# Kernel optimization log

Hardware: AMD Instinct MI355X
Metric: run time of the kernel (lower is better)

## Reference

```python
import jax, jax.numpy as jnp
import numpy as np

EMB = 1024
HEADS = 16
HEAD_DIM = EMB // HEADS


def setup_inputs() -> dict:
    key = jax.random.key(0)
    ks = jax.random.split(key, 12)
    B, S = 4, 2048
    scale = 1.0 / np.sqrt(EMB)
    inp = {
        'values': jax.random.normal(ks[0], (B, S, EMB), jnp.float32),
        'keys': jax.random.normal(ks[1], (B, S, EMB), jnp.float32),
        'query': jax.random.normal(ks[2], (B, S, EMB), jnp.float32),
        'Wv': jax.random.normal(ks[3], (EMB, EMB), jnp.float32) * scale,
        'bv': jnp.zeros((EMB,), jnp.float32),
        'Wk': jax.random.normal(ks[4], (EMB, EMB), jnp.float32) * scale,
        'bk': jnp.zeros((EMB,), jnp.float32),
        'Wq': jax.random.normal(ks[5], (EMB, EMB), jnp.float32) * scale,
        'bq': jnp.zeros((EMB,), jnp.float32),
        'Wo': jax.random.normal(ks[6], (EMB, EMB), jnp.float32) * scale,
        'bo': jnp.zeros((EMB,), jnp.float32),
    }
    return inp


def reference(values, keys, query, Wv, bv, Wk, bk, Wq, bq, Wo, bo):
    B, S, _ = values.shape
    # Linear projections (torch Linear: x @ W.T + b)
    v = values @ Wv.T + bv
    k = keys @ Wk.T + bk
    q = query @ Wq.T + bq
    # Reshape to (B, S, H, D) -- NOTE: original does NOT transpose heads,
    # so attention is computed across the HEAD axis per position.
    v = v.reshape(B, S, HEADS, HEAD_DIM)
    k = k.reshape(B, S, HEADS, HEAD_DIM)
    q = q.reshape(B, S, HEADS, HEAD_DIM)
    # (B,S,H,D) @ (B,S,D,H) -> (B,S,H,H) head-head scores
    scores = jnp.einsum('bshd,bsgd->bshg', q, k) * (HEAD_DIM ** -0.5)
    attn = jax.nn.softmax(scores, axis=-1)
    # (B,S,H,H) @ (B,S,H,D) -> (B,S,H,D)
    out = jnp.einsum('bshg,bsgd->bshd', attn, v)
    out = out.reshape(B, S, EMB)
    return out @ Wo.T + bo
```

## Files before the change

### kernel.cpp

```cpp
#include <hip/hip_runtime.h>
#include <stdint.h>

#define EMB 1024
#define LROW 40

typedef unsigned short u16;
typedef __attribute__((ext_vector_type(8))) unsigned short u16x8;
typedef __attribute__((ext_vector_type(8))) __bf16 bf16x8;
typedef __attribute__((ext_vector_type(4))) float f32x4;

__device__ __forceinline__ u16 f2bf(float f) {
  union { float f; uint32_t u; } x; x.f = f;
  uint32_t u = x.u;
  u += 0x7fff + ((u >> 16) & 1u);
  return (u16)(u >> 16);
}

template<int F32>
__device__ __forceinline__ u16x8 ld8(const void* p, size_t off) {
  if (F32) {
    const float4* f = (const float4*)((const float*)p + off);
    const float4 lo = f[0], hi = f[1];
    u16x8 r;
    r[0] = f2bf(lo.x); r[1] = f2bf(lo.y); r[2] = f2bf(lo.z); r[3] = f2bf(lo.w);
    r[4] = f2bf(hi.x); r[5] = f2bf(hi.y); r[6] = f2bf(hi.z); r[7] = f2bf(hi.w);
    return r;
  }
  return *(const u16x8*)((const u16*)p + off);
}

__device__ __forceinline__ void gl16(const u16* g, u16* l) {
  __builtin_amdgcn_global_load_lds(
      (const __attribute__((address_space(1))) void*)g,
      (__attribute__((address_space(3))) void*)l, 16, 0, 0);
}

__global__ __launch_bounds__(256) void cvt2_kernel(
    const float* __restrict__ a0, u16* __restrict__ b0, int n0,
    const float* __restrict__ a1, u16* __restrict__ b1, int n1)
{
  int i = blockIdx.x * 256 + threadIdx.x;
  const int stride = gridDim.x * 256;
  const int tot = n0 + n1;
  for (; i < tot; i += stride) {
    const float* src; u16* dst; int j;
    if (i < n0) { src = a0; dst = b0; j = i; }
    else        { src = a1; dst = b1; j = i - n0; }
    const float4* f = (const float4*)(src + (size_t)j * 8);
    const float4 lo = f[0], hi = f[1];
    u16x8 r;
    r[0] = f2bf(lo.x); r[1] = f2bf(lo.y); r[2] = f2bf(lo.z); r[3] = f2bf(lo.w);
    r[4] = f2bf(hi.x); r[5] = f2bf(hi.y); r[6] = f2bf(hi.z); r[7] = f2bf(hi.w);
    *(u16x8*)(dst + (size_t)j * 8) = r;
  }
}

template<int CF32>
__device__ __forceinline__ void gemm_lds_core(
    const u16* __restrict__ X, const u16* __restrict__ W,
    const float* __restrict__ Bias, void* __restrict__ C,
    int bm, int bn, int N, int K, u16* Al, u16* Bl)
{
  const int tid  = threadIdx.x;
  const int lane = tid & 63;
  const int w    = tid >> 6;
  const int wm = w >> 1, wn = w & 1;
  const int r16 = lane & 15, quad = lane >> 4;

  const int s0 = w * 64 + lane;
  const int s1 = s0 + 256;
  const int r0 = s0 >> 2, c0 = ((s0 & 3) ^ (r0 & 3)) * 8;
  const int r1 = s1 >> 2, c1 = ((s1 & 3) ^ (r1 & 3)) * 8;

  const u16* srcA0 = X + (size_t)(bm + r0) * K + c0;
  const u16* srcA1 = X + (size_t)(bm + r1) * K + c1;
  const u16* srcB0 = W + (size_t)(bn + r0) * K + c0;
  const u16* srcB1 = W + (size_t)(bn + r1) * K + c1;

  u16* dA0 = Al + (w * 64) * 8;
  u16* dA1 = dA0 + 256 * 8;
  u16* dB0 = Bl + (w * 64) * 8;
  u16* dB1 = dB0 + 256 * 8;

  const int swz = (quad ^ (r16 & 3)) * 8;
  int offA[4], offB[4];
#pragma unroll
  for (int t = 0; t < 4; t++) {
    offA[t] = (wm * 64 + t * 16 + r16) * 32 + swz;
    offB[t] = (wn * 64 + t * 16 + r16) * 32 + swz;
  }

  f32x4 acc[4][4];
#pragma unroll
  for (int i = 0; i < 4; i++)
#pragma unroll
    for (int j = 0; j < 4; j++)
      acc[i][j] = f32x4{0.f, 0.f, 0.f, 0.f};

  for (int k0 = 0; k0 < K; k0 += 32) {
    gl16(srcA0 + k0, dA0);
    gl16(srcA1 + k0, dA1);
    gl16(srcB0 + k0, dB0);
    gl16(srcB1 + k0, dB1);
    __syncthreads();

    bf16x8 a[4], b[4];
#pragma unroll
    for (int t = 0; t < 4; t++) a[t] = *(const bf16x8*)&Al[offA[t]];
#pragma unroll
    for (int t = 0; t < 4; t++) b[t] = *(const bf16x8*)&Bl[offB[t]];

#pragma unroll
    for (int tm = 0; tm < 4; tm++)
#pragma unroll
      for (int tn = 0; tn < 4; tn++)
        acc[tm][tn] = __builtin_amdgcn_mfma_f32_16x16x32_bf16(a[tm], b[tn], acc[tm][tn], 0, 0, 0);
    __syncthreads();
  }

#pragma unroll
  for (int tn = 0; tn < 4; tn++) {
    const int col = bn + wn * 64 + tn * 16 + r16;
    const float bias = Bias[col];
#pragma unroll
    for (int tm = 0; tm < 4; tm++) {
      const int row0 = bm + wm * 64 + tm * 16 + quad * 4;
#pragma unroll
      for (int r = 0; r < 4; r++) {
        const float val = acc[tm][tn][r] + bias;
        const size_t idx = (size_t)(row0 + r) * N + col;
        if (CF32) ((float*)C)[idx] = val;
        else      ((u16*)C)[idx]   = f2bf(val);
      }
    }
  }
}

__global__ __launch_bounds__(256, 3) void gemm_bf16_b16out_kernel(
    const u16* __restrict__ X, const u16* __restrict__ W,
    const float* __restrict__ B, u16* __restrict__ C, int N, int K)
{
  __shared__ __attribute__((aligned(16))) u16 Al[128 * 32];
  __shared__ __attribute__((aligned(16))) u16 Bl[128 * 32];
  gemm_lds_core<0>(X, W, B, C, blockIdx.y * 128, blockIdx.x * 128, N, K, Al, Bl);
}

__global__ __launch_bounds__(256, 3) void gemm_bf16_f32out_kernel(
    const u16* __restrict__ X, const u16* __restrict__ W,
    const float* __restrict__ B, float* __restrict__ C, int N, int K)
{
  __shared__ __attribute__((aligned(16))) u16 Al[128 * 32];
  __shared__ __attribute__((aligned(16))) u16 Bl[128 * 32];
  gemm_lds_core<1>(X, W, B, C, blockIdx.y * 128, blockIdx.x * 128, N, K, Al, Bl);
}

template<int XF32, int CF32>
__device__ __forceinline__ void gemm_core(
    const void* __restrict__ X, const float* __restrict__ W,
    const float* __restrict__ Bias, void* __restrict__ C,
    int bm, int bn, int N, int K, u16* Al, u16* Bl)
{
  const int tid  = threadIdx.x;
  const int lane = tid & 63;
  const int w    = tid >> 6;
  const int wm = w >> 1, wn = w & 1;
  const int r16 = lane & 15, quad = lane >> 4;

  const int s0 = tid, s1 = tid + 256;
  const int r0 = s0 >> 2, k0o = (s0 & 3) * 8;
  const int r1 = s1 >> 2, k1o = (s1 & 3) * 8;
  const int l0 = r0 * LROW + k0o;
  const int l1 = r1 * LROW + k1o;

  const size_t xo0 = (size_t)(bm + r0) * K + k0o;
  const size_t xo1 = (size_t)(bm + r1) * K + k1o;
  const size_t wo0 = (size_t)(bn + r0) * K + k0o;
  const size_t wo1 = (size_t)(bn + r1) * K + k1o;

  f32x4 acc[4][4];
#pragma unroll
  for (int i = 0; i < 4; i++)
#pragma unroll
    for (int j = 0; j < 4; j++)
      acc[i][j] = f32x4{0.f, 0.f, 0.f, 0.f};

  u16x8 xa = ld8<XF32>(X, xo0);
  u16x8 xb = ld8<XF32>(X, xo1);
  u16x8 wa = ld8<1>(W, wo0);
  u16x8 wb = ld8<1>(W, wo1);

  for (int k0 = 0; k0 < K; k0 += 32) {
    *(u16x8*)&Al[l0] = xa;
    *(u16x8*)&Al[l1] = xb;
    *(u16x8*)&Bl[l0] = wa;
    *(u16x8*)&Bl[l1] = wb;
    __syncthreads();

    const int kn = (k0 + 32 < K) ? (k0 + 32) : 0;
    xa = ld8<XF32>(X, xo0 + kn);
    xb = ld8<XF32>(X, xo1 + kn);
    wa = ld8<1>(W, wo0 + kn);
    wb = ld8<1>(W, wo1 + kn);

    bf16x8 a[4], b[4];
#pragma unroll
    for (int t = 0; t < 4; t++)
      a[t] = *(const bf16x8*)&Al[(wm * 64 + t * 16 + r16) * LROW + quad * 8];
#pragma unroll
    for (int t = 0; t < 4; t++)
      b[t] = *(const bf16x8*)&Bl[(wn * 64 + t * 16 + r16) * LROW + quad * 8];

#pragma unroll
    for (int tm = 0; tm < 4; tm++)
#pragma unroll
      for (int tn = 0; tn < 4; tn++)
        acc[tm][tn] = __builtin_amdgcn_mfma_f32_16x16x32_bf16(a[tm], b[tn], acc[tm][tn], 0, 0, 0);
    __syncthreads();
  }

#pragma unroll
  for (int tn = 0; tn < 4; tn++) {
    const int col = bn + wn * 64 + tn * 16 + r16;
    const float bias = Bias[col];
#pragma unroll
    for (int tm = 0; tm < 4; tm++) {
      const int row0 = bm + wm * 64 + tm * 16 + quad * 4;
#pragma unroll
      for (int r = 0; r < 4; r++) {
        const float val = acc[tm][tn][r] + bias;
        const size_t idx = (size_t)(row0 + r) * N + col;
        if (CF32) ((float*)C)[idx] = val;
        else      ((u16*)C)[idx]   = f2bf(val);
      }
    }
  }
}

__global__ __launch_bounds__(256, 2) void gemm_mixed_kernel(
    const u16* X, const float* W, const float* B, u16* C, int N, int K)
{
  __shared__ __attribute__((aligned(16))) u16 Al[128 * LROW];
  __shared__ __attribute__((aligned(16))) u16 Bl[128 * LROW];
  gemm_core<0, 0>(X, W, B, C, blockIdx.y * 128, blockIdx.x * 128, N, K, Al, Bl);
}

__global__ __launch_bounds__(256, 4) void attn_heads_kernel(
    const u16* Q, const u16* Km, const u16* V, u16* O)
{
  __shared__ __attribute__((aligned(16))) u16 P[4][16 * LROW];
  __shared__ __attribute__((aligned(16))) u16 VT[4][64 * LROW];

  const int tid = threadIdx.x, lane = tid & 63, w = tid >> 6;
  const int r16 = lane & 15, quad = lane >> 4;
  const size_t base = ((size_t)blockIdx.x * 4 + w) * EMB;

  const bf16x8 aq0 = *(const bf16x8*)&Q[base + r16 * 64 + quad * 8];
  const bf16x8 aq1 = *(const bf16x8*)&Q[base + r16 * 64 + 32 + quad * 8];
  const bf16x8 bk0 = *(const bf16x8*)&Km[base + r16 * 64 + quad * 8];
  const bf16x8 bk1 = *(const bf16x8*)&Km[base + r16 * 64 + 32 + quad * 8];

  const u16x8 v0 = *(const u16x8*)&V[base + lane * 16];
  const u16x8 v1 = *(const u16x8*)&V[base + lane * 16 + 8];
  const u16x8 z8 = {0, 0, 0, 0, 0, 0, 0, 0};
  *(u16x8*)&VT[w][lane * LROW + 16] = z8;
  *(u16x8*)&VT[w][lane * LROW + 24] = z8;
  const int g = lane >> 2, dbase = (lane & 3) * 16;
#pragma unroll
  for (int i = 0; i < 8; i++) {
    VT[w][(dbase + i) * LROW + g]     = v0[i];
    VT[w][(dbase + 8 + i) * LROW + g] = v1[i];
  }

  f32x4 s = f32x4{0.f, 0.f, 0.f, 0.f};
  s = __builtin_amdgcn_mfma_f32_16x16x32_bf16(aq0, bk0, s, 0, 0, 0);
  s = __builtin_amdgcn_mfma_f32_16x16x32_bf16(aq1, bk1, s, 0, 0, 0);

  float p[4];
#pragma unroll
  for (int r = 0; r < 4; r++) {
    float v = s[r] * 0.125f;
    float m = v;
#pragma unroll
    for (int d = 8; d; d >>= 1) m = fmaxf(m, __shfl_xor(m, d, 16));
    float e = __expf(v - m);
    float sum = e;
#pragma unroll
    for (int d = 8; d; d >>= 1) sum += __shfl_xor(sum, d, 16);
    p[r] = e / sum;
  }

#pragma unroll
  for (int r = 0; r < 4; r++) {
    P[w][(quad * 4 + r) * LROW + r16]      = f2bf(p[r]);
    P[w][(quad * 4 + r) * LROW + 16 + r16] = 0;
  }
  __syncthreads();

  const bf16x8 pa = *(const bf16x8*)&P[w][r16 * LROW + quad * 8];

#pragma unroll
  for (int c = 0; c < 4; c++) {
    const bf16x8 bv = *(const bf16x8*)&VT[w][(c * 16 + r16) * LROW + quad * 8];
    f32x4 o = f32x4{0.f, 0.f, 0.f, 0.f};
    o = __builtin_amdgcn_mfma_f32_16x16x32_bf16(pa, bv, o, 0, 0, 0);
#pragma unroll
    for (int r = 0; r < 4; r++)
      O[base + (size_t)(quad * 4 + r) * 64 + c * 16 + r16] = f2bf(o[r]);
  }
}

extern "C" void kernel_launch(void* const* d_in, const int* in_sizes, int n_in,
                              void* d_out, int out_size, void* d_ws, size_t ws_size,
                              hipStream_t stream)
{
  const float* values = (const float*)d_in[0];
  const float* keys   = (const float*)d_in[1];
  const float* query  = (const float*)d_in[2];
  const float* Wv = (const float*)d_in[3];
  const float* bv = (const float*)d_in[4];
  const float* Wk = (const float*)d_in[5];
  const float* bk = (const float*)d_in[6];
  const float* Wq = (const float*)d_in[7];
  const float* bq = (const float*)d_in[8];
  const float* Wo = (const float*)d_in[9];
  const float* bo = (const float*)d_in[10];

  const int M = in_sizes[0] / EMB;
  const int N = EMB, K = EMB;

  u16* q    = (u16*)d_ws;
  u16* kbuf = q + (size_t)M * EMB;
  u16* v    = (u16*)d_out;
  u16* xbuf = v + (size_t)M * EMB;
  u16* ao   = q;
  u16* wqb  = kbuf;
  u16* wvb  = kbuf + (size_t)EMB * EMB;
  u16* wob  = kbuf;

  const int n8X = M * EMB / 8;
  const int n8W = EMB * EMB / 8;

  dim3 blk(256, 1, 1);
  dim3 cg(2048, 1, 1);
  dim3 gg(N / 128, M / 128, 1);

  hipLaunchKernelGGL(cvt2_kernel, cg, blk, 0, stream, query, xbuf, n8X, Wq, wqb, n8W);
  hipLaunchKernelGGL(gemm_bf16_b16out_kernel, gg, blk, 0, stream, xbuf, wqb, bq, q, N, K);
  hipLaunchKernelGGL(cvt2_kernel, cg, blk, 0, stream, values, xbuf, n8X, Wv, wvb, n8W);
  hipLaunchKernelGGL(gemm_bf16_b16out_kernel, gg, blk, 0, stream, xbuf, wvb, bv, v, N, K);
  hipLaunchKernelGGL(cvt2_kernel, cg, blk, 0, stream, keys, xbuf, n8X,
                     (const float*)nullptr, (u16*)nullptr, 0);
  hipLaunchKernelGGL(gemm_mixed_kernel, gg, blk, 0, stream, xbuf, Wk, bk, kbuf, N, K);
  hipLaunchKernelGGL(attn_heads_kernel, dim3(M / 4, 1, 1), blk, 0, stream, q, kbuf, v, ao);
  hipLaunchKernelGGL(cvt2_kernel, cg, blk, 0, stream, Wo, wob, n8W,
                     (const float*)nullptr, (u16*)nullptr, 0);
  hipLaunchKernelGGL(gemm_bf16_f32out_kernel, gg, blk, 0, stream, ao, wob, bo, (float*)d_out, N, K);
}
```

Baseline: 313.4 us.

## Fuse QKV projections into one launch with in-kernel fp32 activation conversion

Replaces the three separate activation-conversion passes and three projection GEMMs with one weight-conversion kernel and a single QKV GEMM launch (grid z selects V/K/Q). The fused GEMM reads fp32 activations directly and converts them to bf16 while staging into swizzled LDS, and loads bf16 weights through direct global-to-LDS loads. This removes the full bf16 activation round trips through memory and several launches, and triples the GEMM grid for better occupancy. Wo conversion is batched into the same launch when workspace allows. The cost is doubled fp32 activation read bandwidth in the GEMM and extra conversion ALU work in the main loop.

Measured after the change: 298.2 us. -4.9%, faster.

```diff
diff --git a/kernel.cpp b/kernel.cpp
--- a/kernel.cpp
+++ b/kernel.cpp
@@ -16,17 +16,11 @@
   return (u16)(u >> 16);
 }
 
-template<int F32>
-__device__ __forceinline__ u16x8 ld8(const void* p, size_t off) {
-  if (F32) {
-    const float4* f = (const float4*)((const float*)p + off);
-    const float4 lo = f[0], hi = f[1];
-    u16x8 r;
-    r[0] = f2bf(lo.x); r[1] = f2bf(lo.y); r[2] = f2bf(lo.z); r[3] = f2bf(lo.w);
-    r[4] = f2bf(hi.x); r[5] = f2bf(hi.y); r[6] = f2bf(hi.z); r[7] = f2bf(hi.w);
-    return r;
-  }
-  return *(const u16x8*)((const u16*)p + off);
+__device__ __forceinline__ bf16x8 cvt8(float4 a, float4 b) {
+  bf16x8 r;
+  r[0] = (__bf16)a.x; r[1] = (__bf16)a.y; r[2] = (__bf16)a.z; r[3] = (__bf16)a.w;
+  r[4] = (__bf16)b.x; r[5] = (__bf16)b.y; r[6] = (__bf16)b.z; r[7] = (__bf16)b.w;
+  return r;
 }
 
 __device__ __forceinline__ void gl16(const u16* g, u16* l) {
@@ -35,40 +29,138 @@
       (__attribute__((address_space(3))) void*)l, 16, 0, 0);
 }
 
-__global__ __launch_bounds__(256) void cvt2_kernel(
-    const float* __restrict__ a0, u16* __restrict__ b0, int n0,
-    const float* __restrict__ a1, u16* __restrict__ b1, int n1)
-{
-  int i = blockIdx.x * 256 + threadIdx.x;
-  const int stride = gridDim.x * 256;
-  const int tot = n0 + n1;
-  for (; i < tot; i += stride) {
-    const float* src; u16* dst; int j;
-    if (i < n0) { src = a0; dst = b0; j = i; }
-    else        { src = a1; dst = b1; j = i - n0; }
-    const float4* f = (const float4*)(src + (size_t)j * 8);
-    const float4 lo = f[0], hi = f[1];
-    u16x8 r;
-    r[0] = f2bf(lo.x); r[1] = f2bf(lo.y); r[2] = f2bf(lo.z); r[3] = f2bf(lo.w);
-    r[4] = f2bf(hi.x); r[5] = f2bf(hi.y); r[6] = f2bf(hi.z); r[7] = f2bf(hi.w);
-    *(u16x8*)(dst + (size_t)j * 8) = r;
-  }
-}
-
-template<int CF32>
-__device__ __forceinline__ void gemm_lds_core(
-    const u16* __restrict__ X, const u16* __restrict__ W,
-    const float* __restrict__ Bias, void* __restrict__ C,
-    int bm, int bn, int N, int K, u16* Al, u16* Bl)
-{
+__global__ __launch_bounds__(256) void cvtw_kernel(
+    const float* __restrict__ s0, u16* __restrict__ d0,
+    const float* __restrict__ s1, u16* __restrict__ d1,
+    const float* __restrict__ s2, u16* __restrict__ d2,
+    const float* __restrict__ s3, u16* __restrict__ d3)
+{
+  const float* s; u16* d;
+  switch (blockIdx.y) {
+    case 0:  s = s0; d = d0; break;
+    case 1:  s = s1; d = d1; break;
+    case 2:  s = s2; d = d2; break;
+    default: s = s3; d = d3; break;
+  }
+  const size_t i = (size_t)blockIdx.x * 256 + threadIdx.x;
+  const float4* f = (const float4*)(s + i * 8);
+  const float4 lo = f[0], hi = f[1];
+  *(bf16x8*)(d + i * 8) = cvt8(lo, hi);
+}
+
+__global__ __launch_bounds__(256, 3) void qkv_fused_kernel(
+    const float* __restrict__ Vx, const float* __restrict__ Kx,
+    const float* __restrict__ Qx, const u16* __restrict__ Wb,
+    const float* __restrict__ Bv, const float* __restrict__ Bk,
+    const float* __restrict__ Bq,
+    u16* __restrict__ cv, u16* __restrict__ ck, u16* __restrict__ cq,
+    int N, int K)
+{
+  __shared__ __attribute__((aligned(16))) u16 Al[128 * 32];
+  __shared__ __attribute__((aligned(16))) u16 Bl[128 * 32];
+
+  const float* X; const u16* W; const float* Bias; u16* C;
+  switch (blockIdx.z) {
+    case 0:  X = Vx; W = Wb;                   Bias = Bv; C = cv; break;
+    case 1:  X = Kx; W = Wb + EMB * EMB;       Bias = Bk; C = ck; break;
+    default: X = Qx; W = Wb + 2 * EMB * EMB;   Bias = Bq; C = cq; break;
+  }
+
   const int tid  = threadIdx.x;
   const int lane = tid & 63;
   const int w    = tid >> 6;
   const int wm = w >> 1, wn = w & 1;
   const int r16 = lane & 15, quad = lane >> 4;
-
-  const int s0 = w * 64 + lane;
-  const int s1 = s0 + 256;
+  const int bm = blockIdx.y * 128, bn = blockIdx.x * 128;
+
+  const int s0 = tid, s1 = tid + 256;
+  const int r0 = s0 >> 2, c0 = s0 & 3;
+  const int r1 = s1 >> 2, c1 = s1 & 3;
+  const int lA0 = r0 * 32 + ((c0 ^ (r0 & 3)) * 8);
+  const int lA1 = r1 * 32 + ((c1 ^ (r1 & 3)) * 8);
+  const size_t xo0 = (size_t)(bm + r0) * K + c0 * 8;
+  const size_t xo1 = (size_t)(bm + r1) * K + c1 * 8;
+
+  const int bs0 = w * 64 + lane, bs1 = bs0 + 256;
+  const int br0 = bs0 >> 2, bc0 = ((bs0 & 3) ^ (br0 & 3)) * 8;
+  const int br1 = bs1 >> 2, bc1 = ((bs1 & 3) ^ (br1 & 3)) * 8;
+  const u16* srcB0 = W + (size_t)(bn + br0) * K + bc0;
+  const u16* srcB1 = W + (size_t)(bn + br1) * K + bc1;
+  u16* dB0 = Bl + (w * 64) * 8;
+  u16* dB1 = dB0 + 256 * 8;
+
+  const int swz = (quad ^ (r16 & 3)) * 8;
+  int offA[4], offB[4];
+#pragma unroll
+  for (int t = 0; t < 4; t++) {
+    offA[t] = (wm * 64 + t * 16 + r16) * 32 + swz;
+    offB[t] = (wn * 64 + t * 16 + r16) * 32 + swz;
+  }
+
+  f32x4 acc[4][4];
+#pragma unroll
+  for (int i = 0; i < 4; i++)
+#pragma unroll
+    for (int j = 0; j < 4; j++)
+      acc[i][j] = f32x4{0.f, 0.f, 0.f, 0.f};
+
+  float4 xa0 = *(const float4*)(X + xo0), xa1 = *(const float4*)(X + xo0 + 4);
+  float4 xb0 = *(const float4*)(X + xo1), xb1 = *(const float4*)(X + xo1 + 4);
+
+  for (int k0 = 0; k0 < K; k0 += 32) {
+    *(bf16x8*)&Al[lA0] = cvt8(xa0, xa1);
+    *(bf16x8*)&Al[lA1] = cvt8(xb0, xb1);
+    gl16(srcB0 + k0, dB0);
+    gl16(srcB1 + k0, dB1);
+    __syncthreads();
+
+    const int kn = (k0 + 32 < K) ? (k0 + 32) : 0;
+    xa0 = *(const float4*)(X + xo0 + kn); xa1 = *(const float4*)(X + xo0 + kn + 4);
+    xb0 = *(const float4*)(X + xo1 + kn); xb1 = *(const float4*)(X + xo1 + kn + 4);
+
+    bf16x8 a[4], b[4];
+#pragma unroll
+    for (int t = 0; t < 4; t++) a[t] = *(const bf16x8*)&Al[offA[t]];
+#pragma unroll
+    for (int t = 0; t < 4; t++) b[t] = *(const bf16x8*)&Bl[offB[t]];
+
+#pragma unroll
+    for (int tm = 0; tm < 4; tm++)
+#pragma unroll
+      for (int tn = 0; tn < 4; tn++)
+        acc[tm][tn] = __builtin_amdgcn_mfma_f32_16x16x32_bf16(a[tm], b[tn], acc[tm][tn], 0, 0, 0);
+    __syncthreads();
+  }
+
+#pragma unroll
+  for (int tn = 0; tn < 4; tn++) {
+    const int col = bn + wn * 64 + tn * 16 + r16;
+    const float bias = Bias[col];
+#pragma unroll
+    for (int tm = 0; tm < 4; tm++) {
+      const int row0 = bm + wm * 64 + tm * 16 + quad * 4;
+#pragma unroll
+      for (int r = 0; r < 4; r++)
+        C[(size_t)(row0 + r) * N + col] = f2bf(acc[tm][tn][r] + bias);
+    }
+  }
+}
+
+__global__ __launch_bounds__(256, 3) void out_gemm_kernel(
+    const u16* __restrict__ X, const u16* __restrict__ W,
+    const float* __restrict__ Bias, float* __restrict__ C, int N, int K)
+{
+  __shared__ __attribute__((aligned(16))) u16 Al[128 * 32];
+  __shared__ __attribute__((aligned(16))) u16 Bl[128 * 32];
+
+  const int tid  = threadIdx.x;
+  const int lane = tid & 63;
+  const int w    = tid >> 6;
+  const int wm = w >> 1, wn = w & 1;
+  const int r16 = lane & 15, quad = lane >> 4;
+  const int bm = blockIdx.y * 128, bn = blockIdx.x * 128;
+
+  const int s0 = w * 64 + lane, s1 = s0 + 256;
   const int r0 = s0 >> 2, c0 = ((s0 & 3) ^ (r0 & 3)) * 8;
   const int r1 = s1 >> 2, c1 = ((s1 & 3) ^ (r1 & 3)) * 8;
 
@@ -126,122 +218,10 @@
     for (int tm = 0; tm < 4; tm++) {
       const int row0 = bm + wm * 64 + tm * 16 + quad * 4;
 #pragma unroll
-      for (int r = 0; r < 4; r++) {
-        const float val = acc[tm][tn][r] + bias;
-        const size_t idx = (size_t)(row0 + r) * N + col;
-        if (CF32) ((float*)C)[idx] = val;
-        else      ((u16*)C)[idx]   = f2bf(val);
-      }
+      for (int r = 0; r < 4; r++)
+        C[(size_t)(row0 + r) * N + col] = acc[tm][tn][r] + bias;
     }
   }
-}
-
-__global__ __launch_bounds__(256, 3) void gemm_bf16_b16out_kernel(
-    const u16* __restrict__ X, const u16* __restrict__ W,
-    const float* __restrict__ B, u16* __restrict__ C, int N, int K)
-{
-  __shared__ __attribute__((aligned(16))) u16 Al[128 * 32];
-  __shared__ __attribute__((aligned(16))) u16 Bl[128 * 32];
-  gemm_lds_core<0>(X, W, B, C, blockIdx.y * 128, blockIdx.x * 128, N, K, Al, Bl);
-}
-
-__global__ __launch_bounds__(256, 3) void gemm_bf16_f32out_kernel(
-    const u16* __restrict__ X, const u16* __restrict__ W,
-    const float* __restrict__ B, float* __restrict__ C, int N, int K)
-{
-  __shared__ __attribute__((aligned(16))) u16 Al[128 * 32];
-  __shared__ __attribute__((aligned(16))) u16 Bl[128 * 32];
-  gemm_lds_core<1>(X, W, B, C, blockIdx.y * 128, blockIdx.x * 128, N, K, Al, Bl);
-}
-
-template<int XF32, int CF32>
-__device__ __forceinline__ void gemm_core(
-    const void* __restrict__ X, const float* __restrict__ W,
-    const float* __restrict__ Bias, void* __restrict__ C,
-    int bm, int bn, int N, int K, u16* Al, u16* Bl)
-{
-  const int tid  = threadIdx.x;
-  const int lane = tid & 63;
-  const int w    = tid >> 6;
-  const int wm = w >> 1, wn = w & 1;
-  const int r16 = lane & 15, quad = lane >> 4;
-
-  const int s0 = tid, s1 = tid + 256;
-  const int r0 = s0 >> 2, k0o = (s0 & 3) * 8;
-  const int r1 = s1 >> 2, k1o = (s1 & 3) * 8;
-  const int l0 = r0 * LROW + k0o;
-  const int l1 = r1 * LROW + k1o;
-
-  const size_t xo0 = (size_t)(bm + r0) * K + k0o;
-  const size_t xo1 = (size_t)(bm + r1) * K + k1o;
-  const size_t wo0 = (size_t)(bn + r0) * K + k0o;
-  const size_t wo1 = (size_t)(bn + r1) * K + k1o;
-
-  f32x4 acc[4][4];
-#pragma unroll
-  for (int i = 0; i < 4; i++)
-#pragma unroll
-    for (int j = 0; j < 4; j++)
-      acc[i][j] = f32x4{0.f, 0.f, 0.f, 0.f};
-
-  u16x8 xa = ld8<XF32>(X, xo0);
-  u16x8 xb = ld8<XF32>(X, xo1);
-  u16x8 wa = ld8<1>(W, wo0);
-  u16x8 wb = ld8<1>(W, wo1);
-
-  for (int k0 = 0; k0 < K; k0 += 32) {
-    *(u16x8*)&Al[l0] = xa;
-    *(u16x8*)&Al[l1] = xb;
-    *(u16x8*)&Bl[l0] = wa;
-    *(u16x8*)&Bl[l1] = wb;
-    __syncthreads();
-
-    const int kn = (k0 + 32 < K) ? (k0 + 32) : 0;
-    xa = ld8<XF32>(X, xo0 + kn);
-    xb = ld8<XF32>(X, xo1 + kn);
-    wa = ld8<1>(W, wo0 + kn);
-    wb = ld8<1>(W, wo1 + kn);
-
-    bf16x8 a[4], b[4];
-#pragma unroll
-    for (int t = 0; t < 4; t++)
-      a[t] = *(const bf16x8*)&Al[(wm * 64 + t * 16 + r16) * LROW + quad * 8];
-#pragma unroll
-    for (int t = 0; t < 4; t++)
-      b[t] = *(const bf16x8*)&Bl[(wn * 64 + t * 16 + r16) * LROW + quad * 8];
-
-#pragma unroll
-    for (int tm = 0; tm < 4; tm++)
-#pragma unroll
-      for (int tn = 0; tn < 4; tn++)
-        acc[tm][tn] = __builtin_amdgcn_mfma_f32_16x16x32_bf16(a[tm], b[tn], acc[tm][tn], 0, 0, 0);
-    __syncthreads();
-  }
-
-#pragma unroll
-  for (int tn = 0; tn < 4; tn++) {
-    const int col = bn + wn * 64 + tn * 16 + r16;
-    const float bias = Bias[col];
-#pragma unroll
-    for (int tm = 0; tm < 4; tm++) {
-      const int row0 = bm + wm * 64 + tm * 16 + quad * 4;
-#pragma unroll
-      for (int r = 0; r < 4; r++) {
-        const float val = acc[tm][tn][r] + bias;
-        const size_t idx = (size_t)(row0 + r) * N + col;
-        if (CF32) ((float*)C)[idx] = val;
-        else      ((u16*)C)[idx]   = f2bf(val);
-      }
-    }
-  }
-}
-
-__global__ __launch_bounds__(256, 2) void gemm_mixed_kernel(
-    const u16* X, const float* W, const float* B, u16* C, int N, int K)
-{
-  __shared__ __attribute__((aligned(16))) u16 Al[128 * LROW];
-  __shared__ __attribute__((aligned(16))) u16 Bl[128 * LROW];
-  gemm_core<0, 0>(X, W, B, C, blockIdx.y * 128, blockIdx.x * 128, N, K, Al, Bl);
 }
 
 __global__ __launch_bounds__(256, 4) void attn_heads_kernel(
@@ -300,9 +280,9 @@
 
 #pragma unroll
   for (int c = 0; c < 4; c++) {
-    const bf16x8 bv = *(const bf16x8*)&VT[w][(c * 16 + r16) * LROW + quad * 8];
+    const bf16x8 bvv = *(const bf16x8*)&VT[w][(c * 16 + r16) * LROW + quad * 8];
     f32x4 o = f32x4{0.f, 0.f, 0.f, 0.f};
-    o = __builtin_amdgcn_mfma_f32_16x16x32_bf16(pa, bv, o, 0, 0, 0);
+    o = __builtin_amdgcn_mfma_f32_16x16x32_bf16(pa, bvv, o, 0, 0, 0);
 #pragma unroll
     for (int r = 0; r < 4; r++)
       O[base + (size_t)(quad * 4 + r) * 64 + c * 16 + r16] = f2bf(o[r]);
@@ -331,28 +311,27 @@
   u16* q    = (u16*)d_ws;
   u16* kbuf = q + (size_t)M * EMB;
   u16* v    = (u16*)d_out;
-  u16* xbuf = v + (size_t)M * EMB;
+  u16* wb   = v + (size_t)M * EMB;
   u16* ao   = q;
-  u16* wqb  = kbuf;
-  u16* wvb  = kbuf + (size_t)EMB * EMB;
-  u16* wob  = kbuf;
-
-  const int n8X = M * EMB / 8;
-  const int n8W = EMB * EMB / 8;
+
+  const size_t base_ws = (size_t)2 * M * EMB * sizeof(u16);
+  const bool wo_in_ws = ws_size >= base_ws + (size_t)EMB * EMB * sizeof(u16);
+  u16* wob = wo_in_ws ? kbuf + (size_t)M * EMB : kbuf;
 
   dim3 blk(256, 1, 1);
-  dim3 cg(2048, 1, 1);
-  dim3 gg(N / 128, M / 128, 1);
-
-  hipLaunchKernelGGL(cvt2_kernel, cg, blk, 0, stream, query, xbuf, n8X, Wq, wqb, n8W);
-  hipLaunchKernelGGL(gemm_bf16_b16out_kernel, gg, blk, 0, stream, xbuf, wqb, bq, q, N, K);
-  hipLaunchKernelGGL(cvt2_kernel, cg, blk, 0, stream, values, xbuf, n8X, Wv, wvb, n8W);
-  hipLaunchKernelGGL(gemm_bf16_b16out_kernel, gg, blk, 0, stream, xbuf, wvb, bv, v, N, K);
-  hipLaunchKernelGGL(cvt2_kernel, cg, blk, 0, stream, keys, xbuf, n8X,
-                     (const float*)nullptr, (u16*)nullptr, 0);
-  hipLaunchKernelGGL(gemm_mixed_kernel, gg, blk, 0, stream, xbuf, Wk, bk, kbuf, N, K);
-  hipLaunchKernelGGL(attn_heads_kernel, dim3(M / 4, 1, 1), blk, 0, stream, q, kbuf, v, ao);
-  hipLaunchKernelGGL(cvt2_kernel, cg, blk, 0, stream, Wo, wob, n8W,
-                     (const float*)nullptr, (u16*)nullptr, 0);
-  hipLaunchKernelGGL(gemm_bf16_f32out_kernel, gg, blk, 0, stream, ao, wob, bo, (float*)d_out, N, K);
-}
+  dim3 cwg(EMB * EMB / 8 / 256, wo_in_ws ? 4 : 3, 1);
+
+  hipLaunchKernelGGL(cvtw_kernel, cwg, blk, 0, stream,
+                     Wv, wb, Wk, wb + EMB * EMB, Wq, wb + 2 * EMB * EMB, Wo, wob);
+  hipLaunchKernelGGL(qkv_fused_kernel, dim3(N / 128, M / 128, 3), blk, 0, stream,
+                     values, keys, query, wb, bv, bk, bq, v, kbuf, q, N, K);
+  hipLaunchKernelGGL(attn_heads_kernel, dim3(M / 4, 1, 1), blk, 0, stream,
+                     q, kbuf, v, ao);
+  if (!wo_in_ws)
+    hipLaunchKernelGGL(cvtw_kernel, dim3(EMB * EMB / 8 / 256, 1, 1), blk, 0, stream,
+                       Wo, wob, (const float*)nullptr, (u16*)nullptr,
+                       (const float*)nullptr, (u16*)nullptr,
+                       (const float*)nullptr, (u16*)nullptr);
+  hipLaunchKernelGGL(out_gemm_kernel, dim3(N / 128, M / 128, 1), blk, 0, stream,
+                     ao, wob, bo, (float*)d_out, N, K);
+}
```
